# Kernel tuning notes

Hardware: AMD Instinct MI355X
Metric: run time of the kernel (lower is better)

Reference implementation:

```python
import jax, jax.numpy as jnp
import numpy as np

INF = 1.0e6  # 'infinity' for squared EDT; max real value is ~3*128^2 ~ 5e4


def edt_1d_sq(f, axis):
    """One pass of Felzenszwalb separable squared EDT along `axis`.
    d[i] = min_j f[j] + (i - j)^2  (brute-force vectorized lower envelope)."""
    f = jnp.moveaxis(f, axis, -1)
    n = f.shape[-1]
    i = jnp.arange(n, dtype=f.dtype)
    sq = (i[:, None] - i[None, :]) ** 2  # (n, n)
    d = jnp.min(f[..., None, :] + sq, axis=-1)  # (..., n)
    return jnp.moveaxis(d, -1, axis)


def compute_fg_dtm(mask):
    """Euclidean distance transform of foreground (distance to nearest background),
    matching scipy.ndimage.distance_transform_edt applied per batch element on the
    (C, X, Y, Z) mask (C==1 so the channel axis pass is the identity).
    mask: bool (B, 1, X, Y, Z) -> float32 (B, 1, X, Y, Z)."""
    def per_b(m):
        g = jnp.where(m, jnp.float32(INF), jnp.float32(0.0))
        for ax in range(m.ndim):
            g = edt_1d_sq(g, ax)
        return jnp.sqrt(g)
    return jax.lax.map(per_b, mask)


def setup_inputs() -> dict:
    key = jax.random.key(0)
    k1, k2, k3 = jax.random.split(key, 3)
    B, C, X, Y, Z = 2, 2, 128, 128, 128
    return {
        "outputs": jax.random.normal(k1, (B, C, X, Y, Z), dtype=jnp.float32),
        "outputs_dist": jax.random.normal(k2, (B, C, X, Y, Z), dtype=jnp.float32) * 10.0,
        "y": jax.random.randint(k3, (B, 1, X, Y, Z), 0, 2),
        "distance_map_weight": 1.0,
    }


def reference(outputs, outputs_dist, y, distance_map_weight):
    n_pred_ch = outputs.shape[1]
    # MONAI one_hot: (B,1,X,Y,Z) int labels -> (B,C,X,Y,Z) float
    y1h = jnp.moveaxis(jax.nn.one_hot(y[:, 0], n_pred_ch, dtype=outputs.dtype), -1, 1)
    x = outputs[:, 1:]            # foreground logits (B, 1, X, Y, Z)
    t = y1h[:, 1:]                # foreground mask
    od = outputs_dist[:, 1:]
    gt_dis = compute_fg_dtm(t > 0.5)
    # BCE with logits (mean reduction), numerically stable
    loss_ce = jnp.mean(jnp.maximum(x, 0.0) - x * t + jnp.log1p(jnp.exp(-jnp.abs(x))))
    # dice loss, flattened per batch element
    N = x.shape[0]
    smooth = jnp.float32(1.0)
    p = jax.nn.sigmoid(x).reshape(N, -1)
    tf = t.reshape(N, -1)
    dice = (2.0 * jnp.sum(p * tf, axis=1) + smooth) / (jnp.sum(p, axis=1) + jnp.sum(tf, axis=1) + smooth)
    loss_dice = 1.0 - jnp.sum(dice) / N
    # weighted L1 on the distance head, masked by the foreground mask
    msum = jnp.sum(t)
    loss_dist = jnp.where(
        msum == 0,
        jnp.float32(0.0),
        jnp.sum(jnp.abs(od - gt_dis) * t) / jnp.maximum(msum, jnp.float32(1e-12)),
    )
    return loss_ce + loss_dice + distance_map_weight * loss_dist
```

## Files before the change

kernel.cpp:

```cpp
#include <hip/hip_runtime.h>
#include <math.h>

#define M_SPATIAL 2097152
#define MV4 (M_SPATIAL / 4)

__device__ __forceinline__ float wave_redf(float v) {
#pragma unroll
  for (int o = 32; o > 0; o >>= 1) v += __shfl_down(v, o, 64);
  return v;
}
__device__ __forceinline__ double wave_redd(double v) {
#pragma unroll
  for (int o = 32; o > 0; o >>= 1) v += __shfl_down(v, o, 64);
  return v;
}


__global__ __launch_bounds__(256) void kA_ce(const float4* __restrict__ outputs4,
                                             const int4* __restrict__ y4,
                                             double* __restrict__ part) {
  int blk = blockIdx.x;
  int base = blk * 1024;
  int b = (blk >= 512) ? 1 : 0;
  const float4* xc = outputs4 + (size_t)(b * 2 + 1) * MV4;
  float ce = 0.f, ps = 0.f, pts = 0.f, tsum = 0.f;
#pragma unroll
  for (int k = 0; k < 4; ++k) {
    int v4 = base + (int)threadIdx.x + k * 256;
    int s4 = v4 & (MV4 - 1);
    int4 yv = y4[v4];
    float4 x = xc[s4];
#define ELEM(c, yc)                                                         \
    {                                                                       \
      float t = (yc == 1) ? 1.0f : 0.0f;                                    \
      float xx = x.c;                                                       \
      ce += fmaxf(xx, 0.0f) - xx * t + log1pf(expf(-fabsf(xx)));            \
      float p = 1.0f / (1.0f + expf(-xx));                                  \
      ps += p; pts += p * t; tsum += t;                                     \
    }
    ELEM(x, yv.x) ELEM(y, yv.y) ELEM(z, yv.z) ELEM(w, yv.w)
#undef ELEM
  }
  float r0 = wave_redf(ce), r1 = wave_redf(ps), r2 = wave_redf(pts), r3 = wave_redf(tsum);
  __shared__ float sm[4][4];
  int lane = threadIdx.x & 63, w = threadIdx.x >> 6;
  if (lane == 0) { sm[w][0] = r0; sm[w][1] = r1; sm[w][2] = r2; sm[w][3] = r3; }
  __syncthreads();
  if (threadIdx.x == 0) {
    part[blk]        = (double)(sm[0][0] + sm[1][0] + sm[2][0] + sm[3][0]);
    part[1024 + blk] = (double)(sm[0][1] + sm[1][1] + sm[2][1] + sm[3][1]);
    part[2048 + blk] = (double)(sm[0][2] + sm[1][2] + sm[2][2] + sm[3][2]);
    part[3072 + blk] = (double)(sm[0][3] + sm[1][3] + sm[2][3] + sm[3][3]);
  }
}

__global__ __launch_bounds__(256) void kB_edtx(const int* __restrict__ y,
                                               float* __restrict__ g) {
  int blk = blockIdx.x;
  int b  = blk >> 9;
  int yy = (blk >> 2) & 127;
  int zq = blk & 3;
  int t  = threadIdx.x;
  int c  = t >> 5;
  int zl = t & 31;
  int x0 = c * 16;
  size_t base = (size_t)b * M_SPATIAL + (size_t)yy * 128 + (size_t)zq * 32 + zl;

  int yb[16];
#pragma unroll
  for (int k = 0; k < 16; ++k) yb[k] = y[base + (size_t)(x0 + k) * 16384];

  int lastE = -200, nextE = 400;
#pragma unroll
  for (int k = 0; k < 16; ++k) lastE = (yb[k] == 1) ? lastE : (x0 + k);
#pragma unroll
  for (int k = 15; k >= 0; --k) nextE = (yb[k] == 1) ? nextE : (x0 + k);

  __shared__ int lE[8][32];
  __shared__ int nE[8][32];
  lE[c][zl] = lastE;
  nE[c][zl] = nextE;
  __syncthreads();

  int carryL = -200, carryN = 400;
#pragma unroll
  for (int q = 0; q < 7; ++q) {
    if (q < c)     carryL = max(carryL, lE[q][zl]);
    if (q + 1 > c) carryN = min(carryN, nE[q + 1][zl]);
  }

  float yy2f = (float)(yy * yy);
  float hinf = 1000000.f + yy2f;

  int df[16];
  int ll = carryL;
#pragma unroll
  for (int k = 0; k < 16; ++k) {
    ll = (yb[k] == 1) ? ll : (x0 + k);
    df[k] = min(x0 + k - ll, 200);
  }
  float ov[16];
  int nn = carryN;
#pragma unroll
  for (int k = 15; k >= 0; --k) {
    nn = (yb[k] == 1) ? nn : (x0 + k);
    int m = min(df[k], min(nn - (x0 + k), 200));
    ov[k] = (m >= 128) ? hinf : ((float)(m * m) + yy2f);
  }
#pragma unroll
  for (int k = 0; k < 16; ++k) g[base + (size_t)(x0 + k) * 16384] = ov[k];
}

__global__ __launch_bounds__(256) void kC_edty(float* __restrict__ g) {
  __shared__ float hl[128 * 33];
  int blk = blockIdx.x;
  int b = blk >> 9, xx = (blk >> 2) & 127, zc = blk & 3;
  int t = threadIdx.x;
  size_t rb = (size_t)b * M_SPATIAL + (size_t)xx * 16384 + (size_t)zc * 32;

#pragma unroll
  for (int r = 0; r < 4; ++r) {
    int i4 = t + r * 256;
    int j = i4 >> 3, w = i4 & 7;
    float4 v = *(const float4*)(g + rb + (size_t)j * 128 + 4 * w);
    hl[j * 33 + 4 * w + 0] = v.x;
    hl[j * 33 + 4 * w + 1] = v.y;
    hl[j * 33 + 4 * w + 2] = v.z;
    hl[j * 33 + 4 * w + 3] = v.w;
  }
  __syncthreads();

  int zl = t & 31, ig = t >> 5;
  float best[16], mc[16];
#pragma unroll
  for (int k = 0; k < 16; ++k) {
    best[k] = 3.0e38f;
    mc[k] = -2.0f * (float)(ig * 16 + k);
  }
#pragma unroll 2
  for (int j = 0; j < 128; j += 2) {
    float h0 = hl[j * 33 + zl];
    float h1 = hl[(j + 1) * 33 + zl];
    float j0 = (float)j, j1 = (float)(j + 1);
#pragma unroll
    for (int k = 0; k < 16; ++k)
      best[k] = fminf(fminf(fmaf(mc[k], j0, h0), fmaf(mc[k], j1, h1)), best[k]);
  }
  int gz = zc * 32 + zl;
  float zq = (float)(gz * gz);
  size_t ob = rb + zl;
#pragma unroll
  for (int k = 0; k < 16; ++k) {
    int i = ig * 16 + k;
    float dY = (float)(i * i) + best[k];
    g[ob + (size_t)i * 128] = dY + zq;
  }
}

__global__ __launch_bounds__(256) void kD_edtz_dist(const float* __restrict__ g,
                                                    const float* __restrict__ od,
                                                    double* __restrict__ part) {
  __shared__ float hl[128 * 33];
  __shared__ float sred[4];
  int blk = blockIdx.x;
  int b = blk >> 9, xx = (blk >> 2) & 127, yc = blk & 3;
  int t = threadIdx.x;
  size_t rb = (size_t)b * M_SPATIAL + (size_t)xx * 16384 + (size_t)yc * 4096;
  int yl = t & 31, ig = t >> 5;

  size_t odb = (size_t)(2 * b + 1) * M_SPATIAL + (size_t)xx * 16384 +
               (size_t)yc * 4096 + (size_t)yl * 128 + (size_t)ig * 16;
  const float4* o4 = (const float4*)(od + odb);
  float4 ov[4];
#pragma unroll
  for (int r = 0; r < 4; ++r) ov[r] = o4[r];

  const float4* h4 = (const float4*)(g + rb);
#pragma unroll
  for (int r = 0; r < 4; ++r) {
    int i4 = t + r * 256;
    float4 v = h4[i4];
    int flat = i4 * 4;
    int z = flat & 127, yw = flat >> 7;
    hl[(z + 0) * 33 + yw] = v.x;
    hl[(z + 1) * 33 + yw] = v.y;
    hl[(z + 2) * 33 + yw] = v.z;
    hl[(z + 3) * 33 + yw] = v.w;
  }
  __syncthreads();

  float best[16], mc[16];
#pragma unroll
  for (int k = 0; k < 16; ++k) {
    best[k] = 3.0e38f;
    mc[k] = -2.0f * (float)(ig * 16 + k);
  }
#pragma unroll 2
  for (int j = 0; j < 128; j += 2) {
    float h0 = hl[j * 33 + yl];
    float h1 = hl[(j + 1) * 33 + yl];
    float j0 = (float)j, j1 = (float)(j + 1);
#pragma unroll
    for (int k = 0; k < 16; ++k)
      best[k] = fminf(fminf(fmaf(mc[k], j0, h0), fmaf(mc[k], j1, h1)), best[k]);
  }
  const float* of = (const float*)ov;
  float dist = 0.f;
#pragma unroll
  for (int k = 0; k < 16; ++k) {
    int i = ig * 16 + k;
    float dv = (float)(i * i) + best[k];
    if (dv > 0.f) dist += fabsf(of[k] - sqrtf(dv));
  }
  float r = wave_redf(dist);
  int lane = t & 63, w = t >> 6;
  if (lane == 0) sred[w] = r;
  __syncthreads();
  if (t == 0) part[4096 + blk] = (double)(sred[0] + sred[1] + sred[2] + sred[3]);
}

__global__ __launch_bounds__(256) void k_final(const double* __restrict__ part,
                                               const float* __restrict__ wptr,
                                               float* __restrict__ out) {
  int i = threadIdx.x;
  double ce  = part[i] + part[i + 256] + part[i + 512] + part[i + 768];
  double p0  = part[1024 + i] + part[1024 + i + 256];
  double p1  = part[1536 + i] + part[1536 + i + 256];
  double pt0 = part[2048 + i] + part[2048 + i + 256];
  double pt1 = part[2560 + i] + part[2560 + i + 256];
  double t0  = part[3072 + i] + part[3072 + i + 256];
  double t1  = part[3584 + i] + part[3584 + i + 256];
  double ds  = part[4096 + i] + part[4096 + i + 256] + part[4096 + i + 512] + part[4096 + i + 768];

  ce = wave_redd(ce); p0 = wave_redd(p0); p1 = wave_redd(p1);
  pt0 = wave_redd(pt0); pt1 = wave_redd(pt1);
  t0 = wave_redd(t0); t1 = wave_redd(t1); ds = wave_redd(ds);

  __shared__ double sm[4][8];
  int lane = threadIdx.x & 63, w = threadIdx.x >> 6;
  if (lane == 0) {
    sm[w][0] = ce; sm[w][1] = p0; sm[w][2] = p1; sm[w][3] = pt0;
    sm[w][4] = pt1; sm[w][5] = t0; sm[w][6] = t1; sm[w][7] = ds;
  }
  __syncthreads();
  if (threadIdx.x == 0) {
    double a[8];
    for (int q = 0; q < 8; ++q) a[q] = sm[0][q] + sm[1][q] + sm[2][q] + sm[3][q];
    double cem = a[0] / 4194304.0;
    double dice0 = (2.0 * a[3] + 1.0) / (a[1] + a[5] + 1.0);
    double dice1 = (2.0 * a[4] + 1.0) / (a[2] + a[6] + 1.0);
    double ldice = 1.0 - 0.5 * (dice0 + dice1);
    double msum = a[5] + a[6];
    double ldist = (msum == 0.0) ? 0.0 : a[7] / fmax(msum, 1e-12);
    out[0] = (float)(cem + ldice + (double)wptr[0] * ldist);
  }
}

extern "C" void kernel_launch(void* const* d_in, const int* in_sizes, int n_in,
                              void* d_out, int out_size, void* d_ws, size_t ws_size,
                              hipStream_t stream) {
  const float* outputs      = (const float*)d_in[0];
  const float* outputs_dist = (const float*)d_in[1];
  const int*   y            = (const int*)d_in[2];
  const float* wptr         = (const float*)d_in[3];
  float* out = (float*)d_out;

  double* part = (double*)d_ws;
  float* g = (float*)((char*)d_ws + 65536);

  kA_ce<<<1024, 256, 0, stream>>>((const float4*)outputs, (const int4*)y, part);
  kB_edtx<<<1024, 256, 0, stream>>>(y, g);
  kC_edty<<<1024, 256, 0, stream>>>(g);
  kD_edtz_dist<<<1024, 256, 0, stream>>>(g, outputs_dist, part);
  k_final<<<1, 256, 0, stream>>>(part, wptr, out);
}
```

Measured before the change: 166.8 us.

## Fuse CE/dice into EDT-x pass and merge Y/Z EDT passes per slab

Folds the BCE/dice reduction into the x-axis EDT kernel so the label tensor is read only once. It also merges the y and z EDT passes into one kernel that keeps a full 128x128 x-slab in shared memory, which removes a global round trip of the intermediate distance field. In exchange, the merged kernel launches only 256 blocks of 512 threads with about 66KB of shared memory and 32-entry register arrays. That may reduce occupancy and latency hiding on a GPU with 256 CUs. The partial-sum indexing for the distance term drops to 256 entries to match the new block count.

```diff
diff --git a/kernel.cpp b/kernel.cpp
--- a/kernel.cpp
+++ b/kernel.cpp
@@ -2,7 +2,6 @@
 #include <math.h>
 
 #define M_SPATIAL 2097152
-#define MV4 (M_SPATIAL / 4)
 
 __device__ __forceinline__ float wave_redf(float v) {
 #pragma unroll
@@ -16,46 +15,10 @@
 }
 
 
-__global__ __launch_bounds__(256) void kA_ce(const float4* __restrict__ outputs4,
-                                             const int4* __restrict__ y4,
-                                             double* __restrict__ part) {
-  int blk = blockIdx.x;
-  int base = blk * 1024;
-  int b = (blk >= 512) ? 1 : 0;
-  const float4* xc = outputs4 + (size_t)(b * 2 + 1) * MV4;
-  float ce = 0.f, ps = 0.f, pts = 0.f, tsum = 0.f;
-#pragma unroll
-  for (int k = 0; k < 4; ++k) {
-    int v4 = base + (int)threadIdx.x + k * 256;
-    int s4 = v4 & (MV4 - 1);
-    int4 yv = y4[v4];
-    float4 x = xc[s4];
-#define ELEM(c, yc)                                                         \
-    {                                                                       \
-      float t = (yc == 1) ? 1.0f : 0.0f;                                    \
-      float xx = x.c;                                                       \
-      ce += fmaxf(xx, 0.0f) - xx * t + log1pf(expf(-fabsf(xx)));            \
-      float p = 1.0f / (1.0f + expf(-xx));                                  \
-      ps += p; pts += p * t; tsum += t;                                     \
-    }
-    ELEM(x, yv.x) ELEM(y, yv.y) ELEM(z, yv.z) ELEM(w, yv.w)
-#undef ELEM
-  }
-  float r0 = wave_redf(ce), r1 = wave_redf(ps), r2 = wave_redf(pts), r3 = wave_redf(tsum);
-  __shared__ float sm[4][4];
-  int lane = threadIdx.x & 63, w = threadIdx.x >> 6;
-  if (lane == 0) { sm[w][0] = r0; sm[w][1] = r1; sm[w][2] = r2; sm[w][3] = r3; }
-  __syncthreads();
-  if (threadIdx.x == 0) {
-    part[blk]        = (double)(sm[0][0] + sm[1][0] + sm[2][0] + sm[3][0]);
-    part[1024 + blk] = (double)(sm[0][1] + sm[1][1] + sm[2][1] + sm[3][1]);
-    part[2048 + blk] = (double)(sm[0][2] + sm[1][2] + sm[2][2] + sm[3][2]);
-    part[3072 + blk] = (double)(sm[0][3] + sm[1][3] + sm[2][3] + sm[3][3]);
-  }
-}
-
-__global__ __launch_bounds__(256) void kB_edtx(const int* __restrict__ y,
-                                               float* __restrict__ g) {
+__global__ __launch_bounds__(256) void kAB(const int* __restrict__ y,
+                                           const float* __restrict__ outputs,
+                                           float* __restrict__ g,
+                                           double* __restrict__ part) {
   int blk = blockIdx.x;
   int b  = blk >> 9;
   int yy = (blk >> 2) & 127;
@@ -64,11 +27,16 @@
   int c  = t >> 5;
   int zl = t & 31;
   int x0 = c * 16;
-  size_t base = (size_t)b * M_SPATIAL + (size_t)yy * 128 + (size_t)zq * 32 + zl;
+  size_t sp   = (size_t)yy * 128 + (size_t)zq * 32 + zl;
+  size_t base = (size_t)b * M_SPATIAL + sp;
+  const float* xc = outputs + (size_t)(b * 2 + 1) * M_SPATIAL;
 
   int yb[16];
+  float xv[16];
 #pragma unroll
   for (int k = 0; k < 16; ++k) yb[k] = y[base + (size_t)(x0 + k) * 16384];
+#pragma unroll
+  for (int k = 0; k < 16; ++k) xv[k] = xc[sp + (size_t)(x0 + k) * 16384];
 
   int lastE = -200, nextE = 400;
 #pragma unroll
@@ -109,106 +77,106 @@
   }
 #pragma unroll
   for (int k = 0; k < 16; ++k) g[base + (size_t)(x0 + k) * 16384] = ov[k];
-}
-
-__global__ __launch_bounds__(256) void kC_edty(float* __restrict__ g) {
-  __shared__ float hl[128 * 33];
+
+  float ce = 0.f, ps = 0.f, pts = 0.f, tsum = 0.f;
+#pragma unroll
+  for (int k = 0; k < 16; ++k) {
+    float tt = (yb[k] == 1) ? 1.0f : 0.0f;
+    float xx = xv[k];
+    ce += fmaxf(xx, 0.0f) - xx * tt + log1pf(expf(-fabsf(xx)));
+    float p = 1.0f / (1.0f + expf(-xx));
+    ps += p; pts += p * tt; tsum += tt;
+  }
+  float r0 = wave_redf(ce), r1 = wave_redf(ps), r2 = wave_redf(pts), r3 = wave_redf(tsum);
+  __shared__ float sm[4][4];
+  int lane = t & 63, w = t >> 6;
+  if (lane == 0) { sm[w][0] = r0; sm[w][1] = r1; sm[w][2] = r2; sm[w][3] = r3; }
+  __syncthreads();
+  if (t == 0) {
+    part[blk]        = (double)(sm[0][0] + sm[1][0] + sm[2][0] + sm[3][0]);
+    part[1024 + blk] = (double)(sm[0][1] + sm[1][1] + sm[2][1] + sm[3][1]);
+    part[2048 + blk] = (double)(sm[0][2] + sm[1][2] + sm[2][2] + sm[3][2]);
+    part[3072 + blk] = (double)(sm[0][3] + sm[1][3] + sm[2][3] + sm[3][3]);
+  }
+}
+
+__global__ __launch_bounds__(512) void kCD(const float* __restrict__ g,
+                                           const float* __restrict__ od,
+                                           double* __restrict__ part) {
+  __shared__ float sbuf[128 * 132];
+  __shared__ float sred[8];
   int blk = blockIdx.x;
-  int b = blk >> 9, xx = (blk >> 2) & 127, zc = blk & 3;
+  int b = blk >> 7, xx = blk & 127;
   int t = threadIdx.x;
-  size_t rb = (size_t)b * M_SPATIAL + (size_t)xx * 16384 + (size_t)zc * 32;
-
-#pragma unroll
-  for (int r = 0; r < 4; ++r) {
-    int i4 = t + r * 256;
-    int j = i4 >> 3, w = i4 & 7;
-    float4 v = *(const float4*)(g + rb + (size_t)j * 128 + 4 * w);
-    hl[j * 33 + 4 * w + 0] = v.x;
-    hl[j * 33 + 4 * w + 1] = v.y;
-    hl[j * 33 + 4 * w + 2] = v.z;
-    hl[j * 33 + 4 * w + 3] = v.w;
-  }
-  __syncthreads();
-
-  int zl = t & 31, ig = t >> 5;
-  float best[16], mc[16];
-#pragma unroll
-  for (int k = 0; k < 16; ++k) {
+  size_t rb = (size_t)b * M_SPATIAL + (size_t)xx * 16384;
+
+  const float4* g4 = (const float4*)(g + rb);
+#pragma unroll
+  for (int r = 0; r < 8; ++r) {
+    int i4 = t + r * 512;
+    float4 v = g4[i4];
+    int flat = i4 * 4;
+    int ys = flat >> 7, zs = flat & 127;
+    *(float4*)&sbuf[ys * 132 + zs] = v;
+  }
+  __syncthreads();
+
+  {
+    int z = t & 127, ibase = (t >> 7) * 32;
+    float zq = (float)(z * z);
+    float best[32], mc[32];
+#pragma unroll
+    for (int k = 0; k < 32; ++k) {
+      best[k] = 3.0e38f;
+      mc[k] = -2.0f * (float)(ibase + k);
+    }
+#pragma unroll 2
+    for (int j = 0; j < 128; j += 2) {
+      float h0 = sbuf[j * 132 + z];
+      float h1 = sbuf[(j + 1) * 132 + z];
+      float j0 = (float)j, j1 = (float)(j + 1);
+#pragma unroll
+      for (int k = 0; k < 32; ++k)
+        best[k] = fminf(fminf(fmaf(mc[k], j0, h0), fmaf(mc[k], j1, h1)), best[k]);
+    }
+    __syncthreads();
+#pragma unroll
+    for (int k = 0; k < 32; ++k) {
+      int i = ibase + k;
+      float dY = (float)(i * i) + best[k];
+      sbuf[z * 129 + i] = dY + zq;
+    }
+  }
+  __syncthreads();
+
+  int yl = t >> 2, izb = (t & 3) * 32;
+  size_t odb = (size_t)(2 * b + 1) * M_SPATIAL + (size_t)xx * 16384 +
+               (size_t)yl * 128 + (size_t)izb;
+  const float4* o4 = (const float4*)(od + odb);
+  float4 ovv[8];
+#pragma unroll
+  for (int r = 0; r < 8; ++r) ovv[r] = o4[r];
+
+  float best[32], mc[32];
+#pragma unroll
+  for (int k = 0; k < 32; ++k) {
     best[k] = 3.0e38f;
-    mc[k] = -2.0f * (float)(ig * 16 + k);
+    mc[k] = -2.0f * (float)(izb + k);
   }
 #pragma unroll 2
   for (int j = 0; j < 128; j += 2) {
-    float h0 = hl[j * 33 + zl];
-    float h1 = hl[(j + 1) * 33 + zl];
+    float h0 = sbuf[j * 129 + yl];
+    float h1 = sbuf[(j + 1) * 129 + yl];
     float j0 = (float)j, j1 = (float)(j + 1);
 #pragma unroll
-    for (int k = 0; k < 16; ++k)
+    for (int k = 0; k < 32; ++k)
       best[k] = fminf(fminf(fmaf(mc[k], j0, h0), fmaf(mc[k], j1, h1)), best[k]);
   }
-  int gz = zc * 32 + zl;
-  float zq = (float)(gz * gz);
-  size_t ob = rb + zl;
-#pragma unroll
-  for (int k = 0; k < 16; ++k) {
-    int i = ig * 16 + k;
-    float dY = (float)(i * i) + best[k];
-    g[ob + (size_t)i * 128] = dY + zq;
-  }
-}
-
-__global__ __launch_bounds__(256) void kD_edtz_dist(const float* __restrict__ g,
-                                                    const float* __restrict__ od,
-                                                    double* __restrict__ part) {
-  __shared__ float hl[128 * 33];
-  __shared__ float sred[4];
-  int blk = blockIdx.x;
-  int b = blk >> 9, xx = (blk >> 2) & 127, yc = blk & 3;
-  int t = threadIdx.x;
-  size_t rb = (size_t)b * M_SPATIAL + (size_t)xx * 16384 + (size_t)yc * 4096;
-  int yl = t & 31, ig = t >> 5;
-
-  size_t odb = (size_t)(2 * b + 1) * M_SPATIAL + (size_t)xx * 16384 +
-               (size_t)yc * 4096 + (size_t)yl * 128 + (size_t)ig * 16;
-  const float4* o4 = (const float4*)(od + odb);
-  float4 ov[4];
-#pragma unroll
-  for (int r = 0; r < 4; ++r) ov[r] = o4[r];
-
-  const float4* h4 = (const float4*)(g + rb);
-#pragma unroll
-  for (int r = 0; r < 4; ++r) {
-    int i4 = t + r * 256;
-    float4 v = h4[i4];
-    int flat = i4 * 4;
-    int z = flat & 127, yw = flat >> 7;
-    hl[(z + 0) * 33 + yw] = v.x;
-    hl[(z + 1) * 33 + yw] = v.y;
-    hl[(z + 2) * 33 + yw] = v.z;
-    hl[(z + 3) * 33 + yw] = v.w;
-  }
-  __syncthreads();
-
-  float best[16], mc[16];
-#pragma unroll
-  for (int k = 0; k < 16; ++k) {
-    best[k] = 3.0e38f;
-    mc[k] = -2.0f * (float)(ig * 16 + k);
-  }
-#pragma unroll 2
-  for (int j = 0; j < 128; j += 2) {
-    float h0 = hl[j * 33 + yl];
-    float h1 = hl[(j + 1) * 33 + yl];
-    float j0 = (float)j, j1 = (float)(j + 1);
-#pragma unroll
-    for (int k = 0; k < 16; ++k)
-      best[k] = fminf(fminf(fmaf(mc[k], j0, h0), fmaf(mc[k], j1, h1)), best[k]);
-  }
-  const float* of = (const float*)ov;
+  const float* of = (const float*)ovv;
   float dist = 0.f;
 #pragma unroll
-  for (int k = 0; k < 16; ++k) {
-    int i = ig * 16 + k;
+  for (int k = 0; k < 32; ++k) {
+    int i = izb + k;
     float dv = (float)(i * i) + best[k];
     if (dv > 0.f) dist += fabsf(of[k] - sqrtf(dv));
   }
@@ -216,7 +184,12 @@
   int lane = t & 63, w = t >> 6;
   if (lane == 0) sred[w] = r;
   __syncthreads();
-  if (t == 0) part[4096 + blk] = (double)(sred[0] + sred[1] + sred[2] + sred[3]);
+  if (t == 0) {
+    float s = 0.f;
+#pragma unroll
+    for (int q = 0; q < 8; ++q) s += sred[q];
+    part[4096 + blk] = (double)s;
+  }
 }
 
 __global__ __launch_bounds__(256) void k_final(const double* __restrict__ part,
@@ -230,7 +203,7 @@
   double pt1 = part[2560 + i] + part[2560 + i + 256];
   double t0  = part[3072 + i] + part[3072 + i + 256];
   double t1  = part[3584 + i] + part[3584 + i + 256];
-  double ds  = part[4096 + i] + part[4096 + i + 256] + part[4096 + i + 512] + part[4096 + i + 768];
+  double ds  = part[4096 + i];
 
   ce = wave_redd(ce); p0 = wave_redd(p0); p1 = wave_redd(p1);
   pt0 = wave_redd(pt0); pt1 = wave_redd(pt1);
@@ -268,9 +241,7 @@
   double* part = (double*)d_ws;
   float* g = (float*)((char*)d_ws + 65536);
 
-  kA_ce<<<1024, 256, 0, stream>>>((const float4*)outputs, (const int4*)y, part);
-  kB_edtx<<<1024, 256, 0, stream>>>(y, g);
-  kC_edty<<<1024, 256, 0, stream>>>(g);
-  kD_edtz_dist<<<1024, 256, 0, stream>>>(g, outputs_dist, part);
+  kAB<<<1024, 256, 0, stream>>>(y, outputs, g, part);
+  kCD<<<256, 512, 0, stream>>>(g, outputs_dist, part);
   k_final<<<1, 256, 0, stream>>>(part, wptr, out);
 }
```

Result: faster. 160.2 us (-4.0%).
